# Optimization experiments

Measured on AMD Instinct MI355X. Metric: run time of the kernel, lower is better.

The kernel has to match this reference:

```python
import jax, jax.numpy as jnp
import numpy as np

B, T, C, H = 2, 2048, 1024, 16
HD = C // H  # head_dim = 64

def _rope(x, cos, sin):
    # x: [B,H,T,HD]; cos/sin: [T,HD//2]
    x2 = x.reshape(*x.shape[:-1], HD // 2, 2)
    x0, x1 = x2[..., 0], x2[..., 1]
    # complex multiply (x0 + i x1) * (cos + i sin)
    o0 = x0 * cos - x1 * sin
    o1 = x0 * sin + x1 * cos
    return jnp.stack([o0, o1], axis=-1).reshape(x.shape)

def setup_inputs() -> dict:
    key = jax.random.key(0)
    k1, k2, k3 = jax.random.split(key, 3)
    x = jax.random.normal(k1, (B, T, C), dtype=jnp.float32)
    w_qkv = jax.random.normal(k2, (C, 3 * C), dtype=jnp.float32) * (1.0 / np.sqrt(C))
    w_proj = jax.random.normal(k3, (C, C), dtype=jnp.float32) * (1.0 / np.sqrt(C))
    # standard RoPE frequencies: theta_j = 10000^(-2j/HD), angles t*theta_j
    inv_freq = 1.0 / (10000.0 ** (np.arange(0, HD, 2, dtype=np.float32) / HD))  # [HD//2]
    ang = np.arange(T, dtype=np.float32)[:, None] * inv_freq[None, :]           # [T,HD//2]
    return {"x": x, "w_qkv": w_qkv, "w_proj": w_proj,
            "freqs_cos": jnp.asarray(np.cos(ang)), "freqs_sin": jnp.asarray(np.sin(ang))}

def reference(x, w_qkv, w_proj, freqs_cos, freqs_sin):
    qkv = x @ w_qkv                                   # [B,T,3C]
    q, k, v = jnp.split(qkv, 3, axis=-1)
    def heads(t):
        return t.reshape(B, T, H, HD).transpose(0, 2, 1, 3)  # [B,H,T,HD]
    q, k, v = heads(q), heads(k), heads(v)
    q = _rope(q, freqs_cos, freqs_sin)
    k = _rope(k, freqs_cos, freqs_sin)
    scores = jnp.einsum('bhqd,bhkd->bhqk', q, k) * (1.0 / np.sqrt(HD))
    causal = jnp.tril(jnp.ones((T, T), dtype=bool))
    scores = jnp.where(causal, scores, jnp.finfo(scores.dtype).min)
    attn = jax.nn.softmax(scores, axis=-1)
    y = jnp.einsum('bhqk,bhkd->bhqd', attn, v)        # [B,H,T,HD]
    y = y.transpose(0, 2, 1, 3).reshape(B, T, C)
    return y @ w_proj
```

## Files before the change

### kernel.cpp

```cpp
#include <hip/hip_runtime.h>

typedef float  floatx4 __attribute__((ext_vector_type(4)));
typedef _Float16 half8 __attribute__((ext_vector_type(8)));
typedef _Float16 half4v __attribute__((ext_vector_type(4)));
typedef _Float16 half2v __attribute__((ext_vector_type(2)));

__device__ __forceinline__ void gld16(const void* g, void* l) {
    __builtin_amdgcn_global_load_lds(
        (const __attribute__((address_space(1))) void*)g,
        (__attribute__((address_space(3))) void*)l, 16, 0, 0);
}

__global__ __launch_bounds__(256) void conv_x_kernel(const float* __restrict__ x,
                                                     _Float16* __restrict__ xh) {
    int i = blockIdx.x * 256 + threadIdx.x;
    float4 v = ((const float4*)x)[i];
    half4v o = { (_Float16)v.x, (_Float16)v.y, (_Float16)v.z, (_Float16)v.w };
    ((half4v*)xh)[i] = o;
}

__global__ __launch_bounds__(256) void transpose_f32f16(const float* __restrict__ W,
                                                        _Float16* __restrict__ WT,
                                                        int K, int N) {
    __shared__ _Float16 t[64][72];
    int n0 = blockIdx.x * 64, k0 = blockIdx.y * 64;
    int c = threadIdx.x & 63, r4 = threadIdx.x >> 6;
    for (int rr = 0; rr < 64; rr += 4) {
        int k = k0 + rr + r4;
        t[rr + r4][c] = (_Float16)W[(size_t)k * N + n0 + c];
    }
    __syncthreads();
    for (int rr = 0; rr < 64; rr += 4) {
        int n = n0 + rr + r4;
        WT[(size_t)n * K + k0 + c] = t[c][rr + r4];
    }
}

__global__ __launch_bounds__(256) void gemm_tn(const _Float16* __restrict__ A,
                                               const _Float16* __restrict__ BT,
                                               _Float16* __restrict__ Cf16,
                                               float* __restrict__ Cf32,
                                               int M, int N, int K) {
    __shared__ __align__(16) _Float16 sAB[2 * 128 * 32];
    _Float16* sA = sAB;
    _Float16* sB = sAB + 128 * 32;

    const int tid  = threadIdx.x;
    const int wave = tid >> 6, lane = tid & 63;
    const int lrow = lane & 15, quad = lane >> 4;
    const int bm = blockIdx.x * 128, bn = blockIdx.y * 128;
    const int waveM = (wave >> 1) * 64, waveN = (wave & 1) * 64;

    floatx4 acc[4][4] = {};

    const int r0 = tid >> 2,          k80 = (tid & 3) * 8;
    const int r1 = (tid + 256) >> 2,  k81 = ((tid + 256) & 3) * 8;
    _Float16* lA0 = sA + (wave * 64) * 8;
    _Float16* lA1 = sA + (wave * 64 + 256) * 8;
    _Float16* lB0 = sB + (wave * 64) * 8;
    _Float16* lB1 = sB + (wave * 64 + 256) * 8;
    const _Float16* A0 = A + (size_t)(bm + r0) * K + k80;
    const _Float16* A1 = A + (size_t)(bm + r1) * K + k81;
    const _Float16* B0 = BT + (size_t)(bn + r0) * K + k80;
    const _Float16* B1 = BT + (size_t)(bn + r1) * K + k81;

    for (int k0 = 0; k0 < K; k0 += 32) {
        gld16(A0 + k0, lA0);
        gld16(A1 + k0, lA1);
        gld16(B0 + k0, lB0);
        gld16(B1 + k0, lB1);
        __syncthreads();

        half8 aF[4], bF[4];
#pragma unroll
        for (int mt = 0; mt < 4; ++mt)
            aF[mt] = *(const half8*)&sA[(waveM + mt * 16 + lrow) * 32 + quad * 8];
#pragma unroll
        for (int nt = 0; nt < 4; ++nt)
            bF[nt] = *(const half8*)&sB[(waveN + nt * 16 + lrow) * 32 + quad * 8];
#pragma unroll
        for (int mt = 0; mt < 4; ++mt)
#pragma unroll
            for (int nt = 0; nt < 4; ++nt)
                acc[mt][nt] = __builtin_amdgcn_mfma_f32_16x16x32_f16(
                    aF[mt], bF[nt], acc[mt][nt], 0, 0, 0);
        __syncthreads();
    }

    if (Cf16) {
        const int PS = 132;
#pragma unroll
        for (int pass = 0; pass < 4; ++pass) {
            if ((wave >> 1) == (pass >> 1)) {
#pragma unroll
                for (int mt2 = 0; mt2 < 2; ++mt2) {
                    int mt = (pass & 1) * 2 + mt2;
#pragma unroll
                    for (int nt = 0; nt < 4; ++nt)
#pragma unroll
                        for (int r = 0; r < 4; ++r)
                            sAB[(mt2 * 16 + quad * 4 + r) * PS + waveN + nt * 16 + lrow] =
                                (_Float16)acc[mt][nt][r];
                }
            }
            __syncthreads();
            {
                int row = tid >> 3, c0 = (tid & 7) * 16;
                const uint4* src = (const uint4*)&sAB[row * PS + c0];
                uint4 d0 = src[0], d1 = src[1];
                uint4* dst = (uint4*)&Cf16[(size_t)(bm + pass * 32 + row) * N + bn + c0];
                dst[0] = d0; dst[1] = d1;
            }
            __syncthreads();
        }
    } else {
#pragma unroll
        for (int mt = 0; mt < 4; ++mt)
#pragma unroll
            for (int nt = 0; nt < 4; ++nt)
#pragma unroll
                for (int r = 0; r < 4; ++r) {
                    int row = bm + waveM + mt * 16 + quad * 4 + r;
                    int col = bn + waveN + nt * 16 + lrow;
                    Cf32[(size_t)row * N + col] = acc[mt][nt][r];
                }
    }
}

__global__ __launch_bounds__(256) void rope_vt(const _Float16* __restrict__ qkv,
                                               const float* __restrict__ fc,
                                               const float* __restrict__ fs,
                                               _Float16* __restrict__ qh,
                                               _Float16* __restrict__ kh,
                                               _Float16* __restrict__ vt) {
    __shared__ _Float16 s[64][72];
    const int bh = blockIdx.y, b = bh >> 4, h = bh & 15;
    const int t0 = blockIdx.x * 64;
    const int tid = threadIdx.x;

    {
        int c4 = (tid & 15) * 4;
        int j0 = c4 >> 1;
        int rr = tid >> 4;
#pragma unroll
        for (int pass = 0; pass < 4; ++pass) {
            int tt = t0 + pass * 16 + rr;
            const _Float16* src = qkv + (size_t)(b * 2048 + tt) * 3072 + h * 64 + c4;
            float c0 = fc[tt * 32 + j0],     s0 = fs[tt * 32 + j0];
            float c1 = fc[tt * 32 + j0 + 1], s1 = fs[tt * 32 + j0 + 1];
            half4v qv = *(const half4v*)(src);
            half4v kv = *(const half4v*)(src + 1024);
            half4v qo, ko;
            {
                float x0 = (float)qv[0], x1 = (float)qv[1];
                qo[0] = (_Float16)(x0 * c0 - x1 * s0); qo[1] = (_Float16)(x0 * s0 + x1 * c0);
                x0 = (float)qv[2]; x1 = (float)qv[3];
                qo[2] = (_Float16)(x0 * c1 - x1 * s1); qo[3] = (_Float16)(x0 * s1 + x1 * c1);
                x0 = (float)kv[0]; x1 = (float)kv[1];
                ko[0] = (_Float16)(x0 * c0 - x1 * s0); ko[1] = (_Float16)(x0 * s0 + x1 * c0);
                x0 = (float)kv[2]; x1 = (float)kv[3];
                ko[2] = (_Float16)(x0 * c1 - x1 * s1); ko[3] = (_Float16)(x0 * s1 + x1 * c1);
            }
            size_t o = ((size_t)bh * 2048 + tt) * 64 + c4;
            *(half4v*)&qh[o] = qo;
            *(half4v*)&kh[o] = ko;
        }
    }
    {
        int c = tid & 63, r4 = tid >> 6;
        const _Float16* srcv = qkv + 2048 + h * 64;
        for (int rr = 0; rr < 64; rr += 4)
            s[rr + r4][c] = srcv[(size_t)(b * 2048 + t0 + rr + r4) * 3072 + c];
        __syncthreads();
        for (int rr = 0; rr < 64; rr += 4)
            vt[((size_t)bh * 64 + rr + r4) * 2048 + t0 + c] = s[c][rr + r4];
    }
}

__global__ __launch_bounds__(512, 4) void attn_mix(const _Float16* __restrict__ Q,
                                                   const _Float16* __restrict__ Kk,
                                                   const _Float16* __restrict__ Vt,
                                                   _Float16* __restrict__ Y) {
    __shared__ __align__(16) _Float16 sK[2][64 * 64];
    __shared__ __align__(16) _Float16 sV[2][64 * 64];
    __shared__ __align__(16) _Float16 sP[128 * 72];

    const int bh = blockIdx.y, b = bh >> 4, h = bh & 15;
    const int p = blockIdx.x;
    const int qt0 = p, qt1 = 31 - p;
    const int nst = qt1 + 1;
    const int tid = threadIdx.x;
    const int wave = tid >> 6, lane = tid & 63;
    const int lq = lane & 15, quad = lane >> 4;

    const int qglob = (lq < 8 ? qt0 * 64 : qt1 * 64) + wave * 8 + (lq & 7);

    const _Float16* Kbase = Kk + (size_t)bh * 2048 * 64;
    const _Float16* Vbase = Vt + (size_t)bh * 64 * 2048;

    const _Float16 qscale = (_Float16)(0.125f * 1.44269504f);
    half8 qF[2];
    {
        const _Float16* Qp = Q + ((size_t)bh * 2048 + qglob) * 64;
#pragma unroll
        for (int ks = 0; ks < 2; ++ks)
            qF[ks] = (*(const half8*)(Qp + ks * 32 + quad * 8)) * qscale;
    }

    floatx4 O[4] = {};
    float lpart = 0.f;

    auto stage = [&](int bufi, int kt) {
        const _Float16* kb = Kbase + (size_t)kt * 64 * 64;
        const _Float16* vb = Vbase + kt * 64;
        int s = tid;
        int row = s >> 3;
        int ccg = (s & 7) ^ (row & 7);
        gld16(kb + row * 64 + ccg * 8, sK[bufi] + s * 8);
        gld16(vb + (size_t)row * 2048 + ccg * 8, sV[bufi] + s * 8);
    };

    stage(0, 0);
    __syncthreads();

    for (int it = 0; it < nst; ++it) {
        int cur = it & 1;
        if (it + 1 < nst) stage(cur ^ 1, it + 1);
        const _Float16* bK = sK[cur];
        const _Float16* bV = sV[cur];

        floatx4 St[4];
#pragma unroll
        for (int kt4 = 0; kt4 < 4; ++kt4) {
            floatx4 s = { -12.f, -12.f, -12.f, -12.f };
#pragma unroll
            for (int ks = 0; ks < 2; ++ks) {
                half8 kf = *(const half8*)&bK[(kt4 * 16 + lq) * 64 +
                                              (((ks * 4 + quad) ^ (lq & 7)) * 8)];
                s = __builtin_amdgcn_mfma_f32_16x16x32_f16(kf, qF[ks], s, 0, 0, 0);
            }
            St[kt4] = s;
        }
        if (it >= qt0) {
            int keybase = it * 64;
#pragma unroll
            for (int kt4 = 0; kt4 < 4; ++kt4)
#pragma unroll
                for (int r = 0; r < 4; ++r)
                    if (keybase + kt4 * 16 + quad * 4 + r > qglob) St[kt4][r] = -1e30f;
        }
#pragma unroll
        for (int kt4 = 0; kt4 < 4; ++kt4)
#pragma unroll
            for (int r = 0; r < 4; ++r)
                St[kt4][r] = __builtin_amdgcn_exp2f(St[kt4][r]);
        lpart += (St[0][0] + St[0][1] + St[0][2] + St[0][3])
               + (St[1][0] + St[1][1] + St[1][2] + St[1][3])
               + (St[2][0] + St[2][1] + St[2][2] + St[2][3])
               + (St[3][0] + St[3][1] + St[3][2] + St[3][3]);

        _Float16* pw = (_Float16*)&sP[(wave * 16 + lq) * 72];
#pragma unroll
        for (int kt4 = 0; kt4 < 4; ++kt4) {
            half4v pk = { (_Float16)St[kt4][0], (_Float16)St[kt4][1],
                          (_Float16)St[kt4][2], (_Float16)St[kt4][3] };
            *(half4v*)(pw + kt4 * 16 + quad * 4) = pk;
        }
        half8 aP[2];
#pragma unroll
        for (int ks = 0; ks < 2; ++ks)
            aP[ks] = *(const half8*)(pw + ks * 32 + quad * 8);
#pragma unroll
        for (int nt = 0; nt < 4; ++nt)
#pragma unroll
            for (int ks = 0; ks < 2; ++ks) {
                half8 vf = *(const half8*)&bV[(nt * 16 + lq) * 64 +
                                              (((ks * 4 + quad) ^ (lq & 7)) * 8)];
                O[nt] = __builtin_amdgcn_mfma_f32_16x16x32_f16(aP[ks], vf, O[nt], 0, 0, 0);
            }
        __syncthreads();
    }

    float l = lpart;
    l += __shfl_xor(l, 16);
    l += __shfl_xor(l, 32);
    float invl = 1.0f / l;
#pragma unroll
    for (int r = 0; r < 4; ++r) {
        int m = quad * 4 + r;
        float iv = __shfl(invl, (lane & 48) | m);
        int qrow = (m < 8 ? qt0 * 64 : qt1 * 64) + wave * 8 + (m & 7);
        size_t rowoff = ((size_t)b * 2048 + qrow) * 1024 + h * 64;
#pragma unroll
        for (int nt = 0; nt < 4; ++nt)
            Y[rowoff + nt * 16 + lq] = (_Float16)(O[nt][r] * iv);
    }
}

extern "C" void kernel_launch(void* const* d_in, const int* in_sizes, int n_in,
                              void* d_out, int out_size, void* d_ws, size_t ws_size,
                              hipStream_t stream) {
    const float* x     = (const float*)d_in[0];
    const float* wqkv  = (const float*)d_in[1];
    const float* wproj = (const float*)d_in[2];
    const float* fc    = (const float*)d_in[3];
    const float* fs    = (const float*)d_in[4];
    float* out = (float*)d_out;

    char* ws = (char*)d_ws;
    _Float16* xh   = (_Float16*)(ws);
    _Float16* wqT  = (_Float16*)(ws + ((size_t)8  << 20));
    _Float16* wpT  = (_Float16*)(ws + ((size_t)14 << 20));
    _Float16* qkvh = (_Float16*)(ws + ((size_t)16 << 20));
    _Float16* qh   = (_Float16*)(ws + ((size_t)40 << 20));
    _Float16* kh   = (_Float16*)(ws + ((size_t)48 << 20));
    _Float16* vt   = (_Float16*)(ws + ((size_t)56 << 20));
    _Float16* yh   = xh;

    conv_x_kernel<<<4096, 256, 0, stream>>>(x, xh);
    transpose_f32f16<<<dim3(48, 16), 256, 0, stream>>>(wqkv, wqT, 1024, 3072);
    transpose_f32f16<<<dim3(16, 16), 256, 0, stream>>>(wproj, wpT, 1024, 1024);
    gemm_tn<<<dim3(32, 24), 256, 0, stream>>>(xh, wqT, qkvh, nullptr, 4096, 3072, 1024);
    rope_vt<<<dim3(32, 32), 256, 0, stream>>>(qkvh, fc, fs, qh, kh, vt);
    attn_mix<<<dim3(16, 32), 512, 0, stream>>>(qh, kh, vt, yh);
    gemm_tn<<<dim3(32, 8), 256, 0, stream>>>(yh, wpT, nullptr, out, 4096, 1024, 1024);
}
```

Measured before the change: 215.9 us.

## Split attention KV range across blocks with partial-sum reduce kernel

Replaces the paired-query-tile attention kernel (512 threads, double-buffered K/V) with a split-K scheme. Each 256-thread block handles one 64-row query tile over at most 16 key tiles. Upper query tiles are split into two halves whose unnormalized outputs and row sums go to a workspace, and a new reduce kernel combines them. This balances causal work across more, smaller blocks for better occupancy. In exchange it drops the K/V double-buffering, adds partial-output traffic in fp16 and an extra launch.

```diff
diff --git a/kernel.cpp b/kernel.cpp
--- a/kernel.cpp
+++ b/kernel.cpp
@@ -177,57 +177,56 @@
     }
 }
 
-__global__ __launch_bounds__(512, 4) void attn_mix(const _Float16* __restrict__ Q,
-                                                   const _Float16* __restrict__ Kk,
-                                                   const _Float16* __restrict__ Vt,
-                                                   _Float16* __restrict__ Y) {
-    __shared__ __align__(16) _Float16 sK[2][64 * 64];
-    __shared__ __align__(16) _Float16 sV[2][64 * 64];
-    __shared__ __align__(16) _Float16 sP[128 * 72];
-
-    const int bh = blockIdx.y, b = bh >> 4, h = bh & 15;
-    const int p = blockIdx.x;
-    const int qt0 = p, qt1 = 31 - p;
-    const int nst = qt1 + 1;
+__global__ __launch_bounds__(256, 6) void attn_sk(const _Float16* __restrict__ Q,
+                                                  const _Float16* __restrict__ Kk,
+                                                  const _Float16* __restrict__ Vt,
+                                                  _Float16* __restrict__ Y,
+                                                  _Float16* __restrict__ Opart,
+                                                  float* __restrict__ lpart) {
+    __shared__ __align__(16) _Float16 sK[64 * 64];
+    __shared__ __align__(16) _Float16 sV[64 * 64];
+    __shared__ __align__(16) _Float16 sP[64 * 72];
+
+    const int bh = blockIdx.x, b = bh >> 4, h = bh & 15;
+    const int u = blockIdx.y;
+    int qt, k0, k1, slot = 0; bool direct;
+    if (u < 16)              { qt = 16 + u;  k0 = 0;  k1 = 15; direct = false; slot = (qt - 16) * 2; }
+    else { int i = (u - 16) >> 1;
+        if (((u - 16) & 1) == 0) { qt = 15 - i; k0 = 0;  k1 = qt; direct = true; }
+        else                     { qt = 31 - i; k0 = 16; k1 = qt; direct = false; slot = (qt - 16) * 2 + 1; }
+    }
+
     const int tid = threadIdx.x;
     const int wave = tid >> 6, lane = tid & 63;
     const int lq = lane & 15, quad = lane >> 4;
 
-    const int qglob = (lq < 8 ? qt0 * 64 : qt1 * 64) + wave * 8 + (lq & 7);
-
     const _Float16* Kbase = Kk + (size_t)bh * 2048 * 64;
     const _Float16* Vbase = Vt + (size_t)bh * 64 * 2048;
 
     const _Float16 qscale = (_Float16)(0.125f * 1.44269504f);
     half8 qF[2];
     {
-        const _Float16* Qp = Q + ((size_t)bh * 2048 + qglob) * 64;
+        const _Float16* Qp = Q + ((size_t)bh * 2048 + qt * 64 + wave * 16 + lq) * 64;
 #pragma unroll
         for (int ks = 0; ks < 2; ++ks)
             qF[ks] = (*(const half8*)(Qp + ks * 32 + quad * 8)) * qscale;
     }
 
     floatx4 O[4] = {};
-    float lpart = 0.f;
-
-    auto stage = [&](int bufi, int kt) {
+    float lacc = 0.f;
+
+    for (int kt = k0; kt <= k1; ++kt) {
         const _Float16* kb = Kbase + (size_t)kt * 64 * 64;
         const _Float16* vb = Vbase + kt * 64;
-        int s = tid;
-        int row = s >> 3;
-        int ccg = (s & 7) ^ (row & 7);
-        gld16(kb + row * 64 + ccg * 8, sK[bufi] + s * 8);
-        gld16(vb + (size_t)row * 2048 + ccg * 8, sV[bufi] + s * 8);
-    };
-
-    stage(0, 0);
-    __syncthreads();
-
-    for (int it = 0; it < nst; ++it) {
-        int cur = it & 1;
-        if (it + 1 < nst) stage(cur ^ 1, it + 1);
-        const _Float16* bK = sK[cur];
-        const _Float16* bV = sV[cur];
+#pragma unroll
+        for (int hlf = 0; hlf < 2; ++hlf) {
+            int s = tid + hlf * 256;
+            int row = s >> 3;
+            int ccg = (s & 7) ^ (row & 7);
+            gld16(kb + row * 64 + ccg * 8, sK + s * 8);
+            gld16(vb + (size_t)row * 2048 + ccg * 8, sV + s * 8);
+        }
+        __syncthreads();
 
         floatx4 St[4];
 #pragma unroll
@@ -235,29 +234,28 @@
             floatx4 s = { -12.f, -12.f, -12.f, -12.f };
 #pragma unroll
             for (int ks = 0; ks < 2; ++ks) {
-                half8 kf = *(const half8*)&bK[(kt4 * 16 + lq) * 64 +
+                half8 kf = *(const half8*)&sK[(kt4 * 16 + lq) * 64 +
                                               (((ks * 4 + quad) ^ (lq & 7)) * 8)];
                 s = __builtin_amdgcn_mfma_f32_16x16x32_f16(kf, qF[ks], s, 0, 0, 0);
             }
             St[kt4] = s;
         }
-        if (it >= qt0) {
-            int keybase = it * 64;
+        if (kt == qt) {
 #pragma unroll
             for (int kt4 = 0; kt4 < 4; ++kt4)
 #pragma unroll
                 for (int r = 0; r < 4; ++r)
-                    if (keybase + kt4 * 16 + quad * 4 + r > qglob) St[kt4][r] = -1e30f;
+                    if (kt4 * 16 + quad * 4 + r > wave * 16 + lq) St[kt4][r] = -1e30f;
         }
 #pragma unroll
         for (int kt4 = 0; kt4 < 4; ++kt4)
 #pragma unroll
             for (int r = 0; r < 4; ++r)
                 St[kt4][r] = __builtin_amdgcn_exp2f(St[kt4][r]);
-        lpart += (St[0][0] + St[0][1] + St[0][2] + St[0][3])
-               + (St[1][0] + St[1][1] + St[1][2] + St[1][3])
-               + (St[2][0] + St[2][1] + St[2][2] + St[2][3])
-               + (St[3][0] + St[3][1] + St[3][2] + St[3][3]);
+        lacc += (St[0][0] + St[0][1] + St[0][2] + St[0][3])
+              + (St[1][0] + St[1][1] + St[1][2] + St[1][3])
+              + (St[2][0] + St[2][1] + St[2][2] + St[2][3])
+              + (St[3][0] + St[3][1] + St[3][2] + St[3][3]);
 
         _Float16* pw = (_Float16*)&sP[(wave * 16 + lq) * 72];
 #pragma unroll
@@ -274,27 +272,67 @@
         for (int nt = 0; nt < 4; ++nt)
 #pragma unroll
             for (int ks = 0; ks < 2; ++ks) {
-                half8 vf = *(const half8*)&bV[(nt * 16 + lq) * 64 +
+                half8 vf = *(const half8*)&sV[(nt * 16 + lq) * 64 +
                                               (((ks * 4 + quad) ^ (lq & 7)) * 8)];
                 O[nt] = __builtin_amdgcn_mfma_f32_16x16x32_f16(aP[ks], vf, O[nt], 0, 0, 0);
             }
         __syncthreads();
     }
 
-    float l = lpart;
+    float l = lacc;
     l += __shfl_xor(l, 16);
     l += __shfl_xor(l, 32);
-    float invl = 1.0f / l;
-#pragma unroll
-    for (int r = 0; r < 4; ++r) {
-        int m = quad * 4 + r;
-        float iv = __shfl(invl, (lane & 48) | m);
-        int qrow = (m < 8 ? qt0 * 64 : qt1 * 64) + wave * 8 + (m & 7);
-        size_t rowoff = ((size_t)b * 2048 + qrow) * 1024 + h * 64;
-#pragma unroll
-        for (int nt = 0; nt < 4; ++nt)
-            Y[rowoff + nt * 16 + lq] = (_Float16)(O[nt][r] * iv);
-    }
+
+    if (direct) {
+        float invl = 1.0f / l;
+#pragma unroll
+        for (int r = 0; r < 4; ++r) {
+            float iv = __shfl(invl, (lane & 48) | (quad * 4 + r));
+            int q = qt * 64 + wave * 16 + quad * 4 + r;
+            size_t rowoff = ((size_t)b * 2048 + q) * 1024 + h * 64;
+#pragma unroll
+            for (int nt = 0; nt < 4; ++nt)
+                Y[rowoff + nt * 16 + lq] = (_Float16)(O[nt][r] * iv);
+        }
+    } else {
+        int gslot = bh * 32 + slot;
+        _Float16* op = Opart + (size_t)gslot * 4096;
+#pragma unroll
+        for (int r = 0; r < 4; ++r) {
+            int row = wave * 16 + quad * 4 + r;
+#pragma unroll
+            for (int nt = 0; nt < 4; ++nt)
+                op[row * 64 + nt * 16 + lq] = (_Float16)O[nt][r];
+        }
+        if (quad == 0)
+            lpart[gslot * 64 + wave * 16 + lq] = l;
+    }
+}
+
+__global__ __launch_bounds__(256) void attn_reduce(const _Float16* __restrict__ Opart,
+                                                   const float* __restrict__ lpart,
+                                                   _Float16* __restrict__ Y) {
+    const int bh = blockIdx.x, b = bh >> 4, h = bh & 15;
+    const int qx = blockIdx.y, qt = 16 + qx;
+    const int g0 = (bh * 16 + qx) * 2, g1 = g0 + 1;
+    const int t = threadIdx.x;
+    const int row = t >> 2, cs = (t & 3) * 16;
+
+    const _Float16* p0 = Opart + (size_t)g0 * 4096 + row * 64 + cs;
+    const _Float16* p1 = Opart + (size_t)g1 * 4096 + row * 64 + cs;
+    float invl = 1.0f / (lpart[g0 * 64 + row] + lpart[g1 * 64 + row]);
+
+    half8 a0 = *(const half8*)p0, a1 = *(const half8*)(p0 + 8);
+    half8 b0 = *(const half8*)p1, b1 = *(const half8*)(p1 + 8);
+    half8 o0, o1;
+#pragma unroll
+    for (int i = 0; i < 8; ++i) {
+        o0[i] = (_Float16)(((float)a0[i] + (float)b0[i]) * invl);
+        o1[i] = (_Float16)(((float)a1[i] + (float)b1[i]) * invl);
+    }
+    _Float16* y = Y + ((size_t)b * 2048 + qt * 64 + row) * 1024 + h * 64 + cs;
+    *(half8*)y = o0;
+    *(half8*)(y + 8) = o1;
 }
 
 extern "C" void kernel_launch(void* const* d_in, const int* in_sizes, int n_in,
@@ -308,20 +346,23 @@
     float* out = (float*)d_out;
 
     char* ws = (char*)d_ws;
-    _Float16* xh   = (_Float16*)(ws);
-    _Float16* wqT  = (_Float16*)(ws + ((size_t)8  << 20));
-    _Float16* wpT  = (_Float16*)(ws + ((size_t)14 << 20));
-    _Float16* qkvh = (_Float16*)(ws + ((size_t)16 << 20));
-    _Float16* qh   = (_Float16*)(ws + ((size_t)40 << 20));
-    _Float16* kh   = (_Float16*)(ws + ((size_t)48 << 20));
-    _Float16* vt   = (_Float16*)(ws + ((size_t)56 << 20));
-    _Float16* yh   = xh;
+    _Float16* xh    = (_Float16*)(ws);
+    _Float16* wqT   = (_Float16*)(ws + ((size_t)8  << 20));
+    _Float16* wpT   = (_Float16*)(ws + ((size_t)14 << 20));
+    _Float16* qkvh  = (_Float16*)(ws + ((size_t)16 << 20));
+    _Float16* qh    = (_Float16*)(ws + ((size_t)40 << 20));
+    _Float16* kh    = (_Float16*)(ws + ((size_t)48 << 20));
+    _Float16* vt    = (_Float16*)(ws + ((size_t)56 << 20));
+    _Float16* yh    = xh;
+    _Float16* Opart = qkvh;
+    float*    lpartf= (float*)(ws + ((size_t)26 << 20));
 
     conv_x_kernel<<<4096, 256, 0, stream>>>(x, xh);
     transpose_f32f16<<<dim3(48, 16), 256, 0, stream>>>(wqkv, wqT, 1024, 3072);
     transpose_f32f16<<<dim3(16, 16), 256, 0, stream>>>(wproj, wpT, 1024, 1024);
     gemm_tn<<<dim3(32, 24), 256, 0, stream>>>(xh, wqT, qkvh, nullptr, 4096, 3072, 1024);
     rope_vt<<<dim3(32, 32), 256, 0, stream>>>(qkvh, fc, fs, qh, kh, vt);
-    attn_mix<<<dim3(16, 32), 512, 0, stream>>>(qh, kh, vt, yh);
+    attn_sk<<<dim3(32, 48), 256, 0, stream>>>(qh, kh, vt, yh, Opart, lpartf);
+    attn_reduce<<<dim3(32, 16), 256, 0, stream>>>(Opart, lpartf, yh);
     gemm_tn<<<dim3(32, 8), 256, 0, stream>>>(yh, wpT, nullptr, out, 4096, 1024, 1024);
 }
```

Result: faster. 196.7 us (-8.9%).
